# Performance work log

Hardware: AMD Instinct MI355X
Metric: run time of the kernel (lower is better)

## Reference

```python
import jax, jax.numpy as jnp
import numpy as np

V, FN, CIN, HID, PTS = 50000, 100000, 3, 256, 10000
TEMP = 0.1
EPS = 1e-20


def line_mesh_graph(f, Vn):
    # f: [F,3] int triangles. Build the 'line mesh': one node per unique mesh edge.
    fe = jnp.concatenate([f[:, :2], f[:, 1:], f[:, jnp.array([2, 0])]], 0)  # [3F,2]
    fe = jnp.sort(fe, axis=1)
    keys = fe[:, 0] * Vn + fe[:, 1]                       # [3F] unique key per undirected edge
    ukeys, inv = jnp.unique(keys, return_inverse=True)
    edge_node = jnp.stack([ukeys // Vn, ukeys % Vn], -1)  # [E,2] endpoints of each edge-node
    E = ukeys.shape[0]
    feid = inv.reshape(3, -1).T                           # [F,3] edge-node id per face edge
    # line-graph connectivity: edges of the same face are mutual neighbors, plus self-loops
    srcs, dsts = [], []
    for i, j in ((0, 1), (1, 0), (1, 2), (2, 1), (2, 0), (0, 2)):
        srcs.append(feid[:, i]); dsts.append(feid[:, j])
    loop = jnp.arange(E)
    edge = jnp.stack([jnp.concatenate(srcs + [loop]), jnp.concatenate(dsts + [loop])], 0)  # [2,NE]
    return edge, edge_node, keys


def gsn_conv(x, edge, Ws, Wn, b):
    # GSNConv stand-in: self transform + mean-aggregated neighbor transform
    s, d = edge[0], edge[1]
    N = x.shape[0]
    deg = jax.ops.segment_sum(jnp.ones_like(s, x.dtype), d, num_segments=N)
    agg = jax.ops.segment_sum(x[s], d, num_segments=N) / jnp.clip(deg, 1.0)[:, None]
    return x @ Ws + agg @ Wn + b


def gumbel_mask(logits, temperature, num, key):
    U = jax.random.uniform(key, logits.shape)
    g = -jnp.log(-jnp.log(U + EPS) + EPS)
    y = jax.nn.softmax((logits + g) / temperature, -1)[:, 0]  # [E]
    _, ind = jax.lax.top_k(y, num)
    y_hard = jnp.zeros_like(y).at[ind].set(1.0)
    mask = jax.lax.stop_gradient(y_hard - y) + y              # straight-through one-hot
    return mask, y_hard == 1.0


def mesh_collapse(f, keys, pool_edge, Vn):
    # Vectorized replacement of the per-pool-edge python loop: hash-join pooled edge keys
    # against all 3F face-edge keys via sorted search.
    PE = pool_edge.shape[0]
    pool_idx = jnp.arange(Vn, Vn + PE)
    edge_keys = keys.reshape(3, -1).T                     # [F,3] (cols: e01,e12,e20)
    pk = pool_edge[:, 0] * Vn + pool_edge[:, 1]
    order = jnp.argsort(pk); pks = pk[order]
    flat = edge_keys.reshape(-1)
    pos = jnp.clip(jnp.searchsorted(pks, flat), 0, PE - 1)
    found = pks[pos] == flat
    pei = jnp.where(found, pool_idx[order[pos]], -1).reshape(-1, 3)  # pool_edge_idx [F,3]
    fm = found.reshape(-1, 3)
    pen = fm.sum(1)                                       # pool_edge_num per face
    psi = (fm * jnp.arange(3)).sum(1)                     # pool_start_idx per face
    vv = jnp.stack([f[:, 0], pei[:, 0], f[:, 1], pei[:, 1], f[:, 2], pei[:, 2]], -1)
    nf0 = f[pen == 0]
    fv1 = vv[pen == 1]; s1 = psi[pen == 1]
    fv1 = jnp.concatenate([fv1[s1 == 0], jnp.roll(fv1[s1 == 1], -2, 1), jnp.roll(fv1[s1 == 2], 2, 1)], 0)
    nf1 = jnp.concatenate([jnp.stack([fv1[:, 0], fv1[:, 1], fv1[:, 4]], -1),
                           jnp.stack([fv1[:, 1], fv1[:, 2], fv1[:, 4]], -1)], 0)
    fv2 = vv[pen == 2]; s2 = psi[pen == 2]
    fv2 = jnp.concatenate([fv2[s2 == 1], jnp.roll(fv2[s2 == 2], 2, 1), jnp.roll(fv2[s2 == 3], -2, 1)], 0)
    nf2 = jnp.concatenate([jnp.stack([fv2[:, 0], fv2[:, 1], fv2[:, 4]], -1),
                           jnp.stack([fv2[:, 1], fv2[:, 2], fv2[:, 3]], -1),
                           jnp.stack([fv2[:, 1], fv2[:, 3], fv2[:, 4]], -1)], 0)
    fv3 = vv[pen == 3]
    nf3 = jnp.concatenate([jnp.stack([fv3[:, 0], fv3[:, 1], fv3[:, 5]], -1),
                           jnp.stack([fv3[:, 1], fv3[:, 2], fv3[:, 3]], -1),
                           jnp.stack([fv3[:, 1], fv3[:, 3], fv3[:, 5]], -1),
                           jnp.stack([fv3[:, 3], fv3[:, 4], fv3[:, 5]], -1)], 0)
    new_faces = jnp.concatenate([nf0, nf1, nf2, nf3], 0)
    ne = jnp.concatenate([new_faces[:, :2], new_faces[:, 1:], new_faces[:, jnp.array([2, 0])]], 0)
    ai = jnp.arange(Vn + PE)
    ne = jnp.concatenate([jnp.stack([ai, ai], -1), ne], 0)
    return new_faces, ne.T


def setup_inputs():
    key = jax.random.key(0)
    ks = jax.random.split(key, 10)
    s1 = 1.0 / np.sqrt(CIN); s2 = 1.0 / np.sqrt(HID)
    return {
        'input': jax.random.normal(ks[0], (1, V, CIN), jnp.float32),
        'face': jax.random.randint(ks[1], (1, FN, 3), 0, V),
        'coord': jax.random.normal(ks[2], (1, V, 3), jnp.float32),
        'detail_points': jax.random.normal(ks[3], (1, PTS, 3), jnp.float32),
        'div': 5,
        'W1s': jax.random.normal(ks[4], (CIN, HID), jnp.float32) * s1,
        'W1n': jax.random.normal(ks[5], (CIN, HID), jnp.float32) * s1,
        'b1': jnp.zeros((HID,), jnp.float32),
        'W2s': jax.random.normal(ks[6], (HID, 2), jnp.float32) * s2,
        'W2n': jax.random.normal(ks[7], (HID, 2), jnp.float32) * s2,
        'b2': jnp.zeros((2,), jnp.float32),
    }


def reference(input, face, coord, detail_points, div, W1s, W1n, b1, W2s, W2n, b2):
    # B=1 (data-dependent per-sample output sizes make batch stacking only valid then)
    x0, f = input[0], face[0]
    Vn = x0.shape[0]
    edge, edge_node, keys = line_mesh_graph(f, Vn)
    xe = 0.5 * (x0[edge_node[:, 0]] + x0[edge_node[:, 1]])   # edge-node features [E,C]
    h = jax.nn.relu(gsn_conv(xe, edge, W1s, W1n, b1))
    out = jax.nn.sigmoid(gsn_conv(h, edge, W2s, W2n, b2))    # [E,2]
    mask, pool_ind = gumbel_mask(out, TEMP, out.shape[0] // div, jax.random.key(42))
    pool_edge = edge_node[pool_ind]                          # [PE,2]
    new_faces, new_edges = mesh_collapse(f, keys, pool_edge, Vn)
    return edge_node[None], new_faces[None], new_edges[None], mask[None]
```

## Files before the change

### kernel.cpp

```cpp
#include <hip/hip_runtime.h>
#include <stdint.h>

typedef uint32_t u32;
typedef uint64_t u64;

#define VN 50000
#define FN 100000
#define K3F 300000
#define EMAX 300000
#define NB1 1172
#define NBC 98
#define NBH 293
#define NBS 293

#define W_A      0u
#define W_B      300000u
#define W_PA     600000u
#define W_PB     900000u
#define W_RANKU  1200000u
#define W_UKEYS  1500000u
#define W_SEGOFF 1800000u
#define W_FEID   2100004u
#define W_XE     2400004u
#define W_PK     3300004u
#define W_P      3400004u
#define W_Q      4000004u
#define W_Y      4600004u
#define W_YMAP   4900004u
#define W_T64    5200004u
#define W_SEL    5800068u
#define W_SELR   6100068u
#define W_CAT    6400068u
#define W_CATR   6500068u
#define W_NFI    6600068u
#define W_HIST   7800068u
#define W_SUMS   8100100u
#define W_CATH   8104196u
#define W_SCAL   8105220u

#define S_E 0
#define S_NUM 1
#define S_PFX 2
#define S_KREM 3
#define S_TU 4
#define S_R 5
#define S_NF 6
#define S_NEN 7
#define S_O1 8
#define S_O2 9
#define S_O3 10
#define S_RS 16
#define S_GS 24
#define S_GP 32

__device__ __forceinline__ void tf2x32(u32 x0, u32 x1, u32& o0, u32& o1) {
  const u32 ks0 = 0u, ks1 = 42u, ks2 = 0x1BD11BDAu ^ 0u ^ 42u;
  x0 += ks0; x1 += ks1;
#define TFR(r) { x0 += x1; x1 = (x1<<(r))|(x1>>(32-(r))); x1 ^= x0; }
  TFR(13) TFR(15) TFR(26) TFR(6)   x0 += ks1; x1 += ks2 + 1u;
  TFR(17) TFR(29) TFR(16) TFR(24)  x0 += ks2; x1 += ks0 + 2u;
  TFR(13) TFR(15) TFR(26) TFR(6)   x0 += ks0; x1 += ks1 + 3u;
  TFR(17) TFR(29) TFR(16) TFR(24)  x0 += ks1; x1 += ks2 + 4u;
  TFR(13) TFR(15) TFR(26) TFR(6)   x0 += ks2; x1 += ks0 + 5u;
#undef TFR
  o0 = x0; o1 = x1;
}

__global__ void scan_blocks(const u32* __restrict__ in, u32* __restrict__ out,
                            u32* __restrict__ sums, int n) {
  __shared__ u32 lds[256];
  int t = threadIdx.x;
  int base = blockIdx.x*1024 + t*4;
  u32 v[4]; u32 tot = 0;
  for (int k = 0; k < 4; ++k) { v[k] = (base+k < n) ? in[base+k] : 0u; tot += v[k]; }
  lds[t] = tot; __syncthreads();
  for (int o = 1; o < 256; o <<= 1) {
    u32 x = (t >= o) ? lds[t-o] : 0u; __syncthreads();
    lds[t] += x; __syncthreads();
  }
  u32 excl = lds[t] - tot;
  if (t == 255) sums[blockIdx.x] = lds[255];
  u32 run = excl;
  for (int k = 0; k < 4; ++k) { if (base+k < n) out[base+k] = run; run += v[k]; }
}

__global__ void scan_flagblocks(const u32* __restrict__ sk, u32* __restrict__ out,
                                u32* __restrict__ sums, int n) {
  __shared__ u32 lds[256];
  int t = threadIdx.x;
  int base = blockIdx.x*1024 + t*4;
  u32 v[4]; u32 tot = 0;
  for (int k = 0; k < 4; ++k) {
    int i = base + k;
    u32 f = 0;
    if (i < n) f = (i == 0 || sk[i-1] != sk[i]) ? 1u : 0u;
    v[k] = f; tot += f;
  }
  lds[t] = tot; __syncthreads();
  for (int o = 1; o < 256; o <<= 1) {
    u32 x = (t >= o) ? lds[t-o] : 0u; __syncthreads();
    lds[t] += x; __syncthreads();
  }
  u32 excl = lds[t] - tot;
  if (t == 255) sums[blockIdx.x] = lds[255];
  u32 run = excl;
  for (int k = 0; k < 4; ++k) { if (base+k < n) out[base+k] = run; run += v[k]; }
}

__global__ void scan_sums(u32* __restrict__ s, int nb) {
  __shared__ u32 lds[256];
  __shared__ u32 carry;
  int t = threadIdx.x;
  if (t == 0) carry = 0;
  __syncthreads();
  for (int base = 0; base < nb; base += 1024) {
    int idx = base + t*4;
    u32 v[4]; u32 tot = 0;
    for (int k = 0; k < 4; ++k) { v[k] = (idx+k < nb) ? s[idx+k] : 0u; tot += v[k]; }
    lds[t] = tot; __syncthreads();
    for (int o = 1; o < 256; o <<= 1) {
      u32 x = (t >= o) ? lds[t-o] : 0u; __syncthreads();
      lds[t] += x; __syncthreads();
    }
    u32 excl = lds[t] - tot;
    u32 ctot = lds[255];
    u32 c = carry;
    __syncthreads();
    u32 run = c + excl;
    for (int k = 0; k < 4; ++k) { if (idx+k < nb) s[idx+k] = run; run += v[k]; }
    if (t == 0) carry = c + ctot;
    __syncthreads();
  }
}

__global__ void scan64_src(const u32* __restrict__ ymap, const u32* __restrict__ scal,
                           u64* __restrict__ part, u64* __restrict__ sums) {
  __shared__ u64 lds[256];
  int t = threadIdx.x;
  int base = blockIdx.x*1024 + t*4;
  int E = (int)scal[S_E];
  u32 TU = scal[S_TU];
  u64 v[4]; u64 tot = 0;
  for (int k = 0; k < 4; ++k) {
    int e = base + k;
    u64 val = 0;
    if (e < E) {
      u32 u = ymap[e];
      if (u > TU) val = 1ull;
      else if (u == TU) val = 1ull << 32;
    }
    v[k] = val; tot += val;
  }
  lds[t] = tot; __syncthreads();
  for (int o = 1; o < 256; o <<= 1) {
    u64 x = (t >= o) ? lds[t-o] : 0ull; __syncthreads();
    lds[t] += x; __syncthreads();
  }
  u64 excl = lds[t] - tot;
  if (t == 255) sums[blockIdx.x] = lds[255];
  u64 run = excl;
  for (int k = 0; k < 4; ++k) { part[base+k] = run; run += v[k]; }
}

__global__ void scan64_sums(u64* __restrict__ s, int nb) {
  __shared__ u64 lds[256];
  int t = threadIdx.x;
  int idx = t*4;
  u64 v[4]; u64 tot = 0;
  for (int k = 0; k < 4; ++k) { v[k] = (idx+k < nb) ? s[idx+k] : 0ull; tot += v[k]; }
  lds[t] = tot; __syncthreads();
  for (int o = 1; o < 256; o <<= 1) {
    u64 x = (t >= o) ? lds[t-o] : 0ull; __syncthreads();
    lds[t] += x; __syncthreads();
  }
  u64 excl = lds[t] - tot;
  u64 run = excl;
  for (int k = 0; k < 4; ++k) { if (idx+k < nb) s[idx+k] = run; run += v[k]; }
}

__global__ void k_sel2(const u32* __restrict__ ymap, const u64* __restrict__ part,
                       const u64* __restrict__ sums, const u32* __restrict__ scal,
                       u32* __restrict__ sel, u32* __restrict__ selr) {
  int e = blockIdx.x*256 + threadIdx.x;
  if (e >= EMAX) return;
  int E = (int)scal[S_E];
  u32 TU = scal[S_TU], R = scal[S_R];
  u64 pre = part[e] + sums[e>>10];
  u32 GTpre = (u32)pre, TIEpre = (u32)(pre >> 32);
  u32 v = 0;
  if (e < E) {
    u32 u = ymap[e];
    v = (u > TU) || (u == TU && TIEpre < R);
  }
  sel[e] = v ? 1u : 0u;
  selr[e] = GTpre + min(TIEpre, R);
}

__global__ void k_rhist(const u32* __restrict__ keys, u32* __restrict__ hist,
                        int n, int shift, int nb) {
  __shared__ u32 h[256];
  int t = threadIdx.x;
  h[t] = 0; __syncthreads();
  int i = blockIdx.x*256 + t;
  if (i < n) atomicAdd(&h[(keys[i]>>shift)&255u], 1u);
  __syncthreads();
  hist[(u32)t*nb + blockIdx.x] = h[t];
}

__global__ void k_rscat(const u32* __restrict__ keys, const u32* __restrict__ pay,
                        u32* __restrict__ okeys, u32* __restrict__ opay,
                        const u32* __restrict__ hist, const u32* __restrict__ sums,
                        int n, int shift, int nb) {
  __shared__ u64 ball[4][8];
  __shared__ u64 vmask[4];
  int t = threadIdx.x, w = t>>6, lane = t&63;
  int i = blockIdx.x*256 + t;
  bool valid = i < n;
  u32 k = valid ? keys[i] : 0u;
  u32 d = (k>>shift)&255u;
  for (int bit = 0; bit < 8; ++bit) {
    u64 bm = __ballot(valid && ((d>>bit)&1u));
    if (lane == 0) ball[w][bit] = bm;
  }
  u64 vb = __ballot(valid ? 1 : 0);
  if (lane == 0) vmask[w] = vb;
  __syncthreads();
  if (valid) {
    u32 rank = 0;
    for (int ww = 0; ww < w; ++ww) {
      u64 m = vmask[ww];
      for (int bit = 0; bit < 8; ++bit) { u64 bb = ball[ww][bit]; m &= ((d>>bit)&1u) ? bb : ~bb; }
      rank += (u32)__popcll(m);
    }
    u64 m = vmask[w];
    for (int bit = 0; bit < 8; ++bit) { u64 bb = ball[w][bit]; m &= ((d>>bit)&1u) ? bb : ~bb; }
    rank += (u32)__popcll(m & ((1ull<<lane)-1ull));
    u32 h = d*(u32)nb + blockIdx.x;
    u32 pos = hist[h] + sums[h>>10] + rank;
    okeys[pos] = k;
    opay[pos] = pay[i];
  }
}

__global__ void k_keys(const int* __restrict__ face, u32* __restrict__ keys,
                       u32* __restrict__ pay) {
  int i = blockIdx.x*256 + threadIdx.x;
  if (i >= K3F) return;
  int s = i / FN, f = i - s*FN;
  int v0 = face[f*3 + s];
  int v1 = face[f*3 + (s == 2 ? 0 : s+1)];
  int a = min(v0, v1), b = max(v0, v1);
  u32 key = (u32)a * (u32)VN + (u32)b;
  keys[i] = key ^ 0x80000000u;
  pay[i] = (u32)i;
}

__global__ void k_uwrite(const u32* __restrict__ sk, const u32* __restrict__ rankp,
                         const u32* __restrict__ sums, const u32* __restrict__ pay,
                         u32* __restrict__ ukeys, u32* __restrict__ segoff,
                         u32* __restrict__ feid,
                         u32* __restrict__ scal, const int* __restrict__ divp) {
  int p = blockIdx.x*256 + threadIdx.x;
  if (p >= K3F) return;
  u32 cur = sk[p];
  u32 fl = (p == 0 || sk[p-1] != cur) ? 1u : 0u;
  u32 rk = rankp[p] + sums[p>>10];
  if (fl) { ukeys[rk] = cur; segoff[rk] = (u32)p; }
  u32 id = rk - 1u + fl;
  u32 i = pay[p];
  u32 s = i / FN, f = i - s*FN;
  feid[f*3 + s] = id;
  if (p == K3F-1) {
    u32 E = rk + fl;
    scal[S_E] = E; scal[S_NUM] = E / (u32)divp[0];
    segoff[E] = (u32)K3F;
  }
}

__global__ void k_ennode(const u32* __restrict__ ukeys, const u32* __restrict__ scal,
                         const float* __restrict__ x,
                         float* __restrict__ xe, float* __restrict__ dout) {
  int e = blockIdx.x*256 + threadIdx.x;
  if (e >= (int)scal[S_E]) return;
  int k = (int)(ukeys[e] ^ 0x80000000u);
  long long kk = (long long)k;
  long long qq = (kk - (kk < 0 ? (long long)(VN-1) : 0ll)) / VN;
  int q = (int)qq;
  int r = (int)(kk - qq * VN);
  dout[2*e]   = (float)q;
  dout[2*e+1] = (float)r;
  u32 i0 = (u32)(q < 0 ? q + VN : q);
  u32 i1 = (u32)r;
  for (int c = 0; c < 3; ++c) xe[e*3+c] = 0.5f*(x[i0*3+c] + x[i1*3+c]);
}

__global__ void k_pack(const float* __restrict__ W1s, const float* __restrict__ W1n,
                       const float* __restrict__ b1,
                       const float* __restrict__ W2s, const float* __restrict__ W2n,
                       float* __restrict__ pk) {
  int h = threadIdx.x;
  if (h >= 256) return;
  float* p = pk + h*12;
  p[0] = W1s[h]; p[1] = W1s[256+h]; p[2] = W1s[512+h];
  p[3] = W1n[h]; p[4] = W1n[256+h]; p[5] = W1n[512+h];
  p[6] = b1[h];
  p[7] = W2s[2*h]; p[8] = W2s[2*h+1];
  p[9] = W2n[2*h]; p[10] = W2n[2*h+1];
  p[11] = 0.0f;
}

__device__ __forceinline__ void agg_neighbors(int e, u32 st, u32 en,
                                              const u32* __restrict__ pay,
                                              const u32* __restrict__ feid,
                                              const float* __restrict__ v, int stride,
                                              float* acc0, float* acc1, float* acc2) {
  const int sslot[6] = {0,1,1,2,2,0};
  const int dslot[6] = {1,0,2,1,0,2};
  float c0 = 0.f, c1 = 0.f, c2 = 0.f;
  for (int b = 0; b < 6; ++b) {
    int j = dslot[b], isl = sslot[b];
    for (u32 p = st; p < en; ++p) {
      u32 i = pay[p];
      u32 s = i / FN;
      if ((int)s == j) {
        u32 f = i - s*FN;
        u32 u = feid[f*3 + isl];
        c0 += v[u*stride]; c1 += v[u*stride+1]; if (stride == 3) c2 += v[u*stride+2];
      }
    }
  }
  c0 += v[e*stride]; c1 += v[e*stride+1]; if (stride == 3) c2 += v[e*stride+2];
  *acc0 = c0; *acc1 = c1; *acc2 = c2;
}

__global__ void k_l12(const float* __restrict__ xe, const u32* __restrict__ segoff,
                      const u32* __restrict__ pay, const u32* __restrict__ feid,
                      const u32* __restrict__ scal, const float* __restrict__ pk,
                      float* __restrict__ P, float* __restrict__ Q) {
  int e = blockIdx.x*256 + threadIdx.x;
  if (e >= (int)scal[S_E]) return;
  u32 st = segoff[e], en = segoff[e+1];
  float c0, c1, c2;
  agg_neighbors(e, st, en, pay, feid, xe, 3, &c0, &c1, &c2);
  float x0 = xe[e*3], x1 = xe[e*3+1], x2 = xe[e*3+2];
  float dg = (float)(2u*(en - st) + 1u);
  float m0 = c0/dg, m1 = c1/dg, m2 = c2/dg;
  float p0 = 0.f, p1 = 0.f, q0 = 0.f, q1 = 0.f;
#pragma unroll 8
  for (int hh = 0; hh < 256; ++hh) {
    const float* w = pk + hh*12;
    float s1 = x0*w[0] + x1*w[1] + x2*w[2];
    float s2 = m0*w[3] + m1*w[4] + m2*w[5];
    float h = fmaxf(s1 + s2 + w[6], 0.0f);
    p0 += h*w[7];  p1 += h*w[8];
    q0 += h*w[9];  q1 += h*w[10];
  }
  P[2*e] = p0; P[2*e+1] = p1; Q[2*e] = q0; Q[2*e+1] = q1;
}

__global__ void k_scores(const float* __restrict__ P, const float* __restrict__ Q,
                         const u32* __restrict__ segoff, const u32* __restrict__ pay,
                         const u32* __restrict__ feid,
                         const float* __restrict__ b2, const u32* __restrict__ scal,
                         float* __restrict__ Y, u32* __restrict__ ymap) {
  int e = blockIdx.x*256 + threadIdx.x;
  u32 E = scal[S_E];
  if (e >= (int)E) return;
  u32 st = segoff[e], en = segoff[e+1];
  float a0, a1, dummy;
  agg_neighbors(e, st, en, pay, feid, Q, 2, &a0, &a1, &dummy);
  float dg = (float)(2u*(en - st) + 1u);
  float z0 = P[2*e]   + a0/dg + b2[0];
  float z1 = P[2*e+1] + a1/dg + b2[1];
  float l0 = 1.0f/(1.0f + expf(-z0));
  float l1 = 1.0f/(1.0f + expf(-z1));
  u32 g0b, g1b;
  { u32 o0,o1; tf2x32(0u, 2u*(u32)e,      o0, o1); g0b = o0 ^ o1; }
  { u32 o0,o1; tf2x32(0u, 2u*(u32)e + 1u, o0, o1); g1b = o0 ^ o1; }
  float U0 = __uint_as_float((g0b>>9) | 0x3f800000u) - 1.0f;
  float U1 = __uint_as_float((g1b>>9) | 0x3f800000u) - 1.0f;
  float g0 = -logf(-logf(U0 + 1e-20f) + 1e-20f);
  float g1 = -logf(-logf(U1 + 1e-20f) + 1e-20f);
  float A0 = (l0 + g0)/0.1f;
  float A1 = (l1 + g1)/0.1f;
  float mx = fmaxf(A0, A1);
  float e0 = expf(A0-mx), e1 = expf(A1-mx);
  float y = e0/(e0+e1);
  Y[e] = y;
  ymap[e] = __float_as_uint(y) | 0x80000000u;
}

__global__ void k_tkinit(u32* __restrict__ scal, u32* __restrict__ hist) {
  int t = threadIdx.x;
  if (t < 256) hist[t] = 0u;
  if (t == 0) { scal[S_PFX] = 0u; scal[S_KREM] = scal[S_NUM]; }
}

__global__ void k_tkhist(const u32* __restrict__ ymap, const u32* __restrict__ scal,
                         u32* __restrict__ hist, int byte) {
  __shared__ u32 h[256];
  int t = threadIdx.x;
  h[t] = 0u; __syncthreads();
  int E = (int)scal[S_E];
  u32 pfx = scal[S_PFX];
  int base = blockIdx.x*1024;
  for (int k = 0; k < 4; ++k) {
    int e = base + k*256 + t;
    if (e < E) {
      u32 u = ymap[e];
      bool match = (byte == 3) || ((u >> ((byte+1)*8)) == pfx);
      if (match) atomicAdd(&h[(u >> (byte*8)) & 255u], 1u);
    }
  }
  __syncthreads();
  u32 c = h[t];
  if (c) atomicAdd(&hist[t], c);
}

__global__ void k_tksel(u32* __restrict__ scal, u32* __restrict__ hist, int byte) {
  __shared__ u32 s2[256];
  __shared__ u32 chosen_s;
  int t = threadIdx.x;
  u32 v = hist[t];
  hist[t] = 0u;
  s2[t] = v;
  if (t == 0) chosen_s = 0u;
  __syncthreads();
  for (int o = 1; o < 256; o <<= 1) {
    u32 x = (t + o < 256) ? s2[t+o] : 0u; __syncthreads();
    s2[t] += x; __syncthreads();
  }
  u32 krem = scal[S_KREM];
  if (s2[t] >= krem) atomicMax(&chosen_s, (u32)t);
  __syncthreads();
  if (t == 0) {
    u32 chosen = chosen_s;
    u32 sufnext = (chosen < 255u) ? s2[chosen+1] : 0u;
    u32 newkrem = krem - sufnext;
    u32 pfx = (scal[S_PFX] << 8) | chosen;
    scal[S_PFX] = pfx; scal[S_KREM] = newkrem;
    if (byte == 0) { scal[S_TU] = pfx; scal[S_R] = newkrem; }
  }
}

__global__ void k_cat(const u32* __restrict__ feid, const u32* __restrict__ sel,
                      u32* __restrict__ cat) {
  int f = blockIdx.x*256 + threadIdx.x;
  if (f >= FN) return;
  u32 m0 = sel[feid[f*3]], m1 = sel[feid[f*3+1]], m2 = sel[feid[f*3+2]];
  u32 pen = m0 + m1 + m2;
  u32 psi = m1 + 2u*m2;
  u32 c = (pen == 0) ? 0u : (pen == 1) ? (1u+psi) : (pen == 2) ? (3u+psi) : 7u;
  cat[f] = c;
}

__global__ void k_cathist(const u32* __restrict__ cat, u32* __restrict__ ch) {
  __shared__ u32 h[8];
  int t = threadIdx.x;
  if (t < 8) h[t] = 0u;
  __syncthreads();
  int base = blockIdx.x*1024 + t*4;
  for (int k = 0; k < 4; ++k) if (base+k < FN) atomicAdd(&h[cat[base+k]], 1u);
  __syncthreads();
  if (t < 8) ch[(u32)t*NBC + blockIdx.x] = h[t];
}

__global__ void k_catoff(u32* __restrict__ ch, u32* __restrict__ scal) {
  __shared__ u32 lds[256];
  __shared__ u32 ex[1024];
  int t = threadIdx.x;
  u32 v[4]; u32 tot = 0;
  for (int k = 0; k < 4; ++k) {
    int i = t*4 + k;
    u32 x = (i < 8*NBC) ? ch[i] : 0u;
    v[k] = x; tot += x;
  }
  lds[t] = tot; __syncthreads();
  for (int o = 1; o < 256; o <<= 1) {
    u32 x = (t >= o) ? lds[t-o] : 0u; __syncthreads();
    lds[t] += x; __syncthreads();
  }
  u32 excl = lds[t] - tot;
  u32 run = excl;
  for (int k = 0; k < 4; ++k) { ex[t*4+k] = run; run += v[k]; }
  __syncthreads();
  for (int k = 0; k < 4; ++k) {
    int i = t*4 + k;
    if (i < 8*NBC) ch[i] = ex[i];
  }
  if (t == 0) {
    u32 total = lds[255];
    u32 bnd[9];
    for (int c = 0; c < 8; ++c) bnd[c] = ex[c*NBC];
    bnd[8] = total;
    u32 tot8[8];
    for (int c = 0; c < 8; ++c) tot8[c] = bnd[c+1] - bnd[c];
    u32 n0 = tot8[0], n1 = tot8[1]+tot8[2]+tot8[3], n2 = tot8[4]+tot8[5]+tot8[6], n3 = tot8[7];
    u32 NF = n0 + 2u*n1 + 3u*n2 + 4u*n3;
    u32 E = scal[S_E], num = scal[S_NUM];
    u32 NEn = (u32)VN + num + 3u*NF;
    scal[S_NF] = NF; scal[S_NEN] = NEn;
    scal[S_O1] = 2u*E;
    scal[S_O2] = 2u*E + 3u*NF;
    scal[S_O3] = 2u*E + 3u*NF + 2u*NEn;
    u32 RS[8] = {0u, n0,n0,n0, n0+2u*n1, n0+2u*n1, n0+2u*n1, n0+2u*n1+3u*n2};
    u32 GS[8] = {0u, n1,n1,n1, n2,n2,n2, n3};
    u32 GP[8] = {0u, n0,n0,n0, n0+n1, n0+n1, n0+n1, n0+n1+n2};
    for (int i = 0; i < 8; ++i) { scal[S_RS+i] = RS[i]; scal[S_GS+i] = GS[i]; scal[S_GP+i] = GP[i]; }
  }
}

__global__ void k_catrank(const u32* __restrict__ cat, const u32* __restrict__ ch,
                          u32* __restrict__ cr) {
  __shared__ u32 lds[256];
  int t = threadIdx.x;
  int base = blockIdx.x*1024 + t*4;
  u32 cc[4], loc[4];
  u32 cnt[8] = {0,0,0,0,0,0,0,0};
  for (int k = 0; k < 4; ++k) {
    int i = base + k;
    if (i < FN) { u32 c = cat[i]; cc[k] = c; loc[k] = cnt[c]++; }
    else cc[k] = 8u;
  }
  u32 tb[8];
  for (int c = 0; c < 8; ++c) {
    lds[t] = cnt[c]; __syncthreads();
    for (int o = 1; o < 256; o <<= 1) {
      u32 x = (t >= o) ? lds[t-o] : 0u; __syncthreads();
      lds[t] += x; __syncthreads();
    }
    tb[c] = lds[t] - cnt[c];
    __syncthreads();
  }
  for (int k = 0; k < 4; ++k) {
    int i = base + k;
    if (i < FN) { u32 c = cc[k]; cr[i] = ch[c*NBC + blockIdx.x] + tb[c] + loc[k]; }
  }
}

__global__ void k_wfaces(const int* __restrict__ face, const u32* __restrict__ cat,
                         const u32* __restrict__ cr, const u32* __restrict__ feid,
                         const u32* __restrict__ selr, const u32* __restrict__ scal,
                         int* __restrict__ nfi, float* __restrict__ dout) {
  int f = blockIdx.x*256 + threadIdx.x;
  if (f >= FN) return;
  const int nfc[8] = {1,2,2,2,3,3,3,4};
  const int tri[8][4][3] = {
    {{0,2,4},{0,0,0},{0,0,0},{0,0,0}},
    {{0,1,4},{1,2,4},{0,0,0},{0,0,0}},
    {{2,3,0},{3,4,0},{0,0,0},{0,0,0}},
    {{4,5,2},{5,0,2},{0,0,0},{0,0,0}},
    {{0,1,4},{1,2,3},{1,3,4},{0,0,0}},
    {{4,5,2},{5,0,1},{5,1,2},{0,0,0}},
    {{2,3,0},{3,4,5},{3,5,0},{0,0,0}},
    {{0,1,5},{1,2,3},{1,3,5},{3,4,5}}};
  u32 c = cat[f];
  int cv[6];
  cv[0] = face[f*3];   cv[2] = face[f*3+1]; cv[4] = face[f*3+2];
  cv[1] = VN + (int)selr[feid[f*3]];
  cv[3] = VN + (int)selr[feid[f*3+1]];
  cv[5] = VN + (int)selr[feid[f*3+2]];
  u32 g  = cr[f] - scal[S_GP + c];
  u32 o1 = scal[S_O1];
  for (int j = 0; j < nfc[c]; ++j) {
    u32 row = scal[S_RS + c] + (u32)j*scal[S_GS + c] + g;
    for (int m = 0; m < 3; ++m) {
      int v = cv[tri[c][j][m]];
      nfi[row*3 + m] = v;
      dout[o1 + row*3 + m] = (float)v;
    }
  }
}

__global__ void k_wne(const int* __restrict__ nfi, const u32* __restrict__ scal,
                      float* __restrict__ dout) {
  int i = blockIdx.x*256 + threadIdx.x;
  u32 NEn = scal[S_NEN];
  if (i >= (int)NEn) return;
  u32 NF = scal[S_NF];
  u32 Vp = (u32)VN + scal[S_NUM];
  u32 o2 = scal[S_O2];
  int a, b;
  if ((u32)i < Vp) { a = i; b = i; }
  else {
    u32 j = (u32)i - Vp;
    u32 blk = j / NF, r = j - blk*NF;
    int i0 = (blk == 0) ? 0 : (blk == 1) ? 1 : 2;
    int i1 = (blk == 0) ? 1 : (blk == 1) ? 2 : 0;
    a = nfi[r*3 + i0]; b = nfi[r*3 + i1];
  }
  dout[o2 + i] = (float)a;
  dout[o2 + NEn + i] = (float)b;
}

__global__ void k_wmask(const u32* __restrict__ sel, const float* __restrict__ Y,
                        const u32* __restrict__ scal, float* __restrict__ dout) {
  int e = blockIdx.x*256 + threadIdx.x;
  if (e >= (int)scal[S_E]) return;
  float y = Y[e];
  float yh = sel[e] ? 1.0f : 0.0f;
  dout[scal[S_O3] + e] = (yh - y) + y;
}

static void radix_pass(u32* kin, u32* pin, u32* kout, u32* pout, u32* hist, u32* sums,
                       int n, int nb, int shift, hipStream_t st) {
  k_rhist<<<nb, 256, 0, st>>>(kin, hist, n, shift, nb);
  int nscan = nb*256;
  int nbs = (nscan + 1023)/1024;
  scan_blocks<<<nbs, 256, 0, st>>>(hist, hist, sums, nscan);
  scan_sums<<<1, 256, 0, st>>>(sums, nbs);
  k_rscat<<<nb, 256, 0, st>>>(kin, pin, kout, pout, hist, sums, n, shift, nb);
}

extern "C" void kernel_launch(void* const* d_in, const int* in_sizes, int n_in,
                              void* d_out, int out_size, void* d_ws, size_t ws_size,
                              hipStream_t stream) {
  const float* x    = (const float*)d_in[0];
  const int*   face = (const int*)d_in[1];
  const int*   divp = (const int*)d_in[4];
  const float* W1s  = (const float*)d_in[5];
  const float* W1n  = (const float*)d_in[6];
  const float* b1   = (const float*)d_in[7];
  const float* W2s  = (const float*)d_in[8];
  const float* W2n  = (const float*)d_in[9];
  const float* b2   = (const float*)d_in[10];
  float* out = (float*)d_out;
  u32* W = (u32*)d_ws;

  u32 *A = W+W_A, *B = W+W_B, *PA = W+W_PA, *PB = W+W_PB;
  u32 *RK = W+W_RANKU, *UK = W+W_UKEYS;
  u32 *HIST = W+W_HIST, *SUMS = W+W_SUMS, *SCAL = W+W_SCAL;
  u64 *T64 = (u64*)(W+W_T64);
  u64 *SUMS64 = (u64*)(W+W_SUMS);

  k_pack<<<1, 256, 0, stream>>>(W1s, W1n, b1, W2s, W2n, (float*)(W+W_PK));

  k_keys<<<NB1, 256, 0, stream>>>(face, A, PA);
  radix_pass(A, PA, B, PB, HIST, SUMS, K3F, NB1,  0, stream);
  radix_pass(B, PB, A, PA, HIST, SUMS, K3F, NB1,  8, stream);
  radix_pass(A, PA, B, PB, HIST, SUMS, K3F, NB1, 16, stream);
  radix_pass(B, PB, A, PA, HIST, SUMS, K3F, NB1, 24, stream);
  scan_flagblocks<<<NBS, 256, 0, stream>>>(A, RK, SUMS, K3F);
  scan_sums<<<1, 256, 0, stream>>>(SUMS, NBS);
  k_uwrite<<<NB1, 256, 0, stream>>>(A, RK, SUMS, PA, UK, W+W_SEGOFF, W+W_FEID, SCAL, divp);

  k_ennode<<<NB1, 256, 0, stream>>>(UK, SCAL, x, (float*)(W+W_XE), out);

  k_l12<<<NB1, 256, 0, stream>>>((float*)(W+W_XE), W+W_SEGOFF, PA, W+W_FEID, SCAL,
                                 (float*)(W+W_PK), (float*)(W+W_P), (float*)(W+W_Q));
  k_scores<<<NB1, 256, 0, stream>>>((float*)(W+W_P), (float*)(W+W_Q), W+W_SEGOFF, PA,
                                    W+W_FEID, b2, SCAL, (float*)(W+W_Y), W+W_YMAP);

  k_tkinit<<<1, 256, 0, stream>>>(SCAL, HIST);
  for (int byte = 3; byte >= 0; --byte) {
    k_tkhist<<<NBH, 256, 0, stream>>>(W+W_YMAP, SCAL, HIST, byte);
    k_tksel<<<1, 256, 0, stream>>>(SCAL, HIST, byte);
  }
  scan64_src<<<NBS, 256, 0, stream>>>(W+W_YMAP, SCAL, T64, SUMS64);
  scan64_sums<<<1, 256, 0, stream>>>(SUMS64, NBS);
  k_sel2<<<NB1, 256, 0, stream>>>(W+W_YMAP, T64, SUMS64, SCAL, W+W_SEL, W+W_SELR);

  k_cat<<<391, 256, 0, stream>>>(W+W_FEID, W+W_SEL, W+W_CAT);
  k_cathist<<<NBC, 256, 0, stream>>>(W+W_CAT, W+W_CATH);
  k_catoff<<<1, 256, 0, stream>>>(W+W_CATH, SCAL);
  k_catrank<<<NBC, 256, 0, stream>>>(W+W_CAT, W+W_CATH, W+W_CATR);
  k_wfaces<<<391, 256, 0, stream>>>(face, W+W_CAT, W+W_CATR, W+W_FEID, W+W_SELR, SCAL,
                                    (int*)(W+W_NFI), out);
  k_wne<<<5118, 256, 0, stream>>>((int*)(W+W_NFI), SCAL, out);
  k_wmask<<<NB1, 256, 0, stream>>>(W+W_SEL, (float*)(W+W_Y), SCAL, out);
}
```

Measured before the change: 329.2 us.

## Pack radix keys with payloads and fuse small kernels to cut launches

Keys and payload indices are packed into one 64-bit word, so each radix scatter does a single store instead of two. The first pass histogram moves into the key-generation kernel, which also absorbs the weight packing. Edge-node feature computation moves into the unique-write kernel. The top-k histogram and select kernels merge into one per round using a last-block-done atomic counter, and the category and category-histogram kernels are fused. This removes many small launches and extra passes, at the cost of 64-bit memory traffic in the sort and a grid-wide completion counter that relies on threadfence ordering.

```diff
diff --git a/kernel.cpp b/kernel.cpp
--- a/kernel.cpp
+++ b/kernel.cpp
@@ -13,30 +13,29 @@
 #define NBH 293
 #define NBS 293
 
-#define W_A      0u
-#define W_B      300000u
-#define W_PA     600000u
-#define W_PB     900000u
+#define W_KPA    0u
+#define W_KPB    600000u
 #define W_RANKU  1200000u
-#define W_UKEYS  1500000u
-#define W_SEGOFF 1800000u
-#define W_FEID   2100004u
-#define W_XE     2400004u
-#define W_PK     3300004u
-#define W_P      3400004u
-#define W_Q      4000004u
-#define W_Y      4600004u
-#define W_YMAP   4900004u
-#define W_T64    5200004u
-#define W_SEL    5800068u
-#define W_SELR   6100068u
-#define W_CAT    6400068u
-#define W_CATR   6500068u
-#define W_NFI    6600068u
-#define W_HIST   7800068u
-#define W_SUMS   8100100u
-#define W_CATH   8104196u
-#define W_SCAL   8105220u
+#define W_SEGOFF 1500000u
+#define W_FEID   1800004u
+#define W_XE     2100004u
+#define W_PK     3000004u
+#define W_P      3100004u
+#define W_Q      3700004u
+#define W_Y      4300004u
+#define W_YMAP   4600004u
+#define W_T64    4900004u
+#define W_SEL    5500068u
+#define W_SELR   5800068u
+#define W_CAT    6100068u
+#define W_CATR   6200068u
+#define W_NFI    6300068u
+#define W_HIST   7500068u
+#define W_SUMS   7800100u
+#define W_CATH   7804196u
+#define W_TKH    7805220u
+#define W_DONE   7805476u
+#define W_SCAL   7805504u
 
 #define S_E 0
 #define S_NUM 1
@@ -84,7 +83,7 @@
   for (int k = 0; k < 4; ++k) { if (base+k < n) out[base+k] = run; run += v[k]; }
 }
 
-__global__ void scan_flagblocks(const u32* __restrict__ sk, u32* __restrict__ out,
+__global__ void scan_flagblocks(const u64* __restrict__ kp, u32* __restrict__ out,
                                 u32* __restrict__ sums, int n) {
   __shared__ u32 lds[256];
   int t = threadIdx.x;
@@ -93,7 +92,7 @@
   for (int k = 0; k < 4; ++k) {
     int i = base + k;
     u32 f = 0;
-    if (i < n) f = (i == 0 || sk[i-1] != sk[i]) ? 1u : 0u;
+    if (i < n) f = (i == 0 || (u32)(kp[i-1]>>32) != (u32)(kp[i]>>32)) ? 1u : 0u;
     v[k] = f; tot += f;
   }
   lds[t] = tot; __syncthreads();
@@ -196,28 +195,27 @@
   selr[e] = GTpre + min(TIEpre, R);
 }
 
-__global__ void k_rhist(const u32* __restrict__ keys, u32* __restrict__ hist,
-                        int n, int shift, int nb) {
+__global__ void k_rhist(const u64* __restrict__ kp, u32* __restrict__ hist,
+                        int shift, int nb) {
   __shared__ u32 h[256];
   int t = threadIdx.x;
   h[t] = 0; __syncthreads();
   int i = blockIdx.x*256 + t;
-  if (i < n) atomicAdd(&h[(keys[i]>>shift)&255u], 1u);
+  if (i < K3F) atomicAdd(&h[((u32)(kp[i]>>32) >> shift) & 255u], 1u);
   __syncthreads();
   hist[(u32)t*nb + blockIdx.x] = h[t];
 }
 
-__global__ void k_rscat(const u32* __restrict__ keys, const u32* __restrict__ pay,
-                        u32* __restrict__ okeys, u32* __restrict__ opay,
+__global__ void k_rscat(const u64* __restrict__ kp, u64* __restrict__ okp,
                         const u32* __restrict__ hist, const u32* __restrict__ sums,
-                        int n, int shift, int nb) {
+                        int shift, int nb) {
   __shared__ u64 ball[4][8];
   __shared__ u64 vmask[4];
   int t = threadIdx.x, w = t>>6, lane = t&63;
   int i = blockIdx.x*256 + t;
-  bool valid = i < n;
-  u32 k = valid ? keys[i] : 0u;
-  u32 d = (k>>shift)&255u;
+  bool valid = i < K3F;
+  u64 v = valid ? kp[i] : 0ull;
+  u32 d = ((u32)(v>>32) >> shift) & 255u;
   for (int bit = 0; bit < 8; ++bit) {
     u64 bm = __ballot(valid && ((d>>bit)&1u));
     if (lane == 0) ball[w][bit] = bm;
@@ -237,80 +235,86 @@
     rank += (u32)__popcll(m & ((1ull<<lane)-1ull));
     u32 h = d*(u32)nb + blockIdx.x;
     u32 pos = hist[h] + sums[h>>10] + rank;
-    okeys[pos] = k;
-    opay[pos] = pay[i];
-  }
-}
-
-__global__ void k_keys(const int* __restrict__ face, u32* __restrict__ keys,
-                       u32* __restrict__ pay) {
-  int i = blockIdx.x*256 + threadIdx.x;
-  if (i >= K3F) return;
-  int s = i / FN, f = i - s*FN;
-  int v0 = face[f*3 + s];
-  int v1 = face[f*3 + (s == 2 ? 0 : s+1)];
-  int a = min(v0, v1), b = max(v0, v1);
-  u32 key = (u32)a * (u32)VN + (u32)b;
-  keys[i] = key ^ 0x80000000u;
-  pay[i] = (u32)i;
-}
-
-__global__ void k_uwrite(const u32* __restrict__ sk, const u32* __restrict__ rankp,
-                         const u32* __restrict__ sums, const u32* __restrict__ pay,
-                         u32* __restrict__ ukeys, u32* __restrict__ segoff,
-                         u32* __restrict__ feid,
+    okp[pos] = v;
+  }
+}
+
+__global__ void k_keys(const int* __restrict__ face,
+                       const float* __restrict__ W1s, const float* __restrict__ W1n,
+                       const float* __restrict__ b1,
+                       const float* __restrict__ W2s, const float* __restrict__ W2n,
+                       float* __restrict__ pk,
+                       u64* __restrict__ kp, u32* __restrict__ hist,
+                       u32* __restrict__ tkh, u32* __restrict__ done) {
+  __shared__ u32 h[256];
+  int t = threadIdx.x;
+  h[t] = 0;
+  __syncthreads();
+  if (blockIdx.x == 0) {
+    tkh[t] = 0u;
+    if (t < 16) done[t] = 0u;
+    float* p = pk + t*12;
+    p[0] = W1s[t]; p[1] = W1s[256+t]; p[2] = W1s[512+t];
+    p[3] = W1n[t]; p[4] = W1n[256+t]; p[5] = W1n[512+t];
+    p[6] = b1[t];
+    p[7] = W2s[2*t]; p[8] = W2s[2*t+1];
+    p[9] = W2n[2*t]; p[10] = W2n[2*t+1];
+    p[11] = 0.0f;
+  }
+  int i = blockIdx.x*256 + t;
+  if (i < K3F) {
+    int s = i / FN, f = i - s*FN;
+    int v0 = face[f*3 + s];
+    int v1 = face[f*3 + (s == 2 ? 0 : s+1)];
+    int a = min(v0, v1), b = max(v0, v1);
+    u32 key = ((u32)a * (u32)VN + (u32)b) ^ 0x80000000u;
+    kp[i] = ((u64)key << 32) | (u32)i;
+    atomicAdd(&h[key & 255u], 1u);
+  }
+  __syncthreads();
+  hist[(u32)t*NB1 + blockIdx.x] = h[t];
+}
+
+__global__ void k_uwrite(const u64* __restrict__ kp, const u32* __restrict__ rankp,
+                         const u32* __restrict__ sums, const float* __restrict__ x,
+                         u32* __restrict__ segoff, u32* __restrict__ feid,
+                         float* __restrict__ xe, float* __restrict__ dout,
                          u32* __restrict__ scal, const int* __restrict__ divp) {
   int p = blockIdx.x*256 + threadIdx.x;
   if (p >= K3F) return;
-  u32 cur = sk[p];
-  u32 fl = (p == 0 || sk[p-1] != cur) ? 1u : 0u;
+  u64 v = kp[p];
+  u32 cur = (u32)(v >> 32);
+  u32 fl = (p == 0 || (u32)(kp[p-1] >> 32) != cur) ? 1u : 0u;
   u32 rk = rankp[p] + sums[p>>10];
-  if (fl) { ukeys[rk] = cur; segoff[rk] = (u32)p; }
+  if (fl) {
+    u32 e = rk;
+    segoff[e] = (u32)p;
+    int k = (int)(cur ^ 0x80000000u);
+    long long kk = (long long)k;
+    long long qq = (kk - (kk < 0 ? (long long)(VN-1) : 0ll)) / VN;
+    int q = (int)qq;
+    int r = (int)(kk - qq * VN);
+    dout[2*e]   = (float)q;
+    dout[2*e+1] = (float)r;
+    u32 i0 = (u32)(q < 0 ? q + VN : q);
+    u32 i1 = (u32)r;
+    for (int c = 0; c < 3; ++c) xe[e*3+c] = 0.5f*(x[i0*3+c] + x[i1*3+c]);
+  }
   u32 id = rk - 1u + fl;
-  u32 i = pay[p];
+  u32 i = (u32)v;
   u32 s = i / FN, f = i - s*FN;
   feid[f*3 + s] = id;
   if (p == K3F-1) {
     u32 E = rk + fl;
-    scal[S_E] = E; scal[S_NUM] = E / (u32)divp[0];
+    u32 num = E / (u32)divp[0];
+    scal[S_E] = E; scal[S_NUM] = num;
     segoff[E] = (u32)K3F;
-  }
-}
-
-__global__ void k_ennode(const u32* __restrict__ ukeys, const u32* __restrict__ scal,
-                         const float* __restrict__ x,
-                         float* __restrict__ xe, float* __restrict__ dout) {
-  int e = blockIdx.x*256 + threadIdx.x;
-  if (e >= (int)scal[S_E]) return;
-  int k = (int)(ukeys[e] ^ 0x80000000u);
-  long long kk = (long long)k;
-  long long qq = (kk - (kk < 0 ? (long long)(VN-1) : 0ll)) / VN;
-  int q = (int)qq;
-  int r = (int)(kk - qq * VN);
-  dout[2*e]   = (float)q;
-  dout[2*e+1] = (float)r;
-  u32 i0 = (u32)(q < 0 ? q + VN : q);
-  u32 i1 = (u32)r;
-  for (int c = 0; c < 3; ++c) xe[e*3+c] = 0.5f*(x[i0*3+c] + x[i1*3+c]);
-}
-
-__global__ void k_pack(const float* __restrict__ W1s, const float* __restrict__ W1n,
-                       const float* __restrict__ b1,
-                       const float* __restrict__ W2s, const float* __restrict__ W2n,
-                       float* __restrict__ pk) {
-  int h = threadIdx.x;
-  if (h >= 256) return;
-  float* p = pk + h*12;
-  p[0] = W1s[h]; p[1] = W1s[256+h]; p[2] = W1s[512+h];
-  p[3] = W1n[h]; p[4] = W1n[256+h]; p[5] = W1n[512+h];
-  p[6] = b1[h];
-  p[7] = W2s[2*h]; p[8] = W2s[2*h+1];
-  p[9] = W2n[2*h]; p[10] = W2n[2*h+1];
-  p[11] = 0.0f;
+    scal[S_PFX] = 0u; scal[S_KREM] = num;
+  }
 }
 
 __device__ __forceinline__ void agg_neighbors(int e, u32 st, u32 en,
-                                              const u32* __restrict__ pay,
+                                              const u64* __restrict__ kp,
                                               const u32* __restrict__ feid,
                                               const float* __restrict__ v, int stride,
                                               float* acc0, float* acc1, float* acc2) {
@@ -320,7 +324,7 @@
   for (int b = 0; b < 6; ++b) {
     int j = dslot[b], isl = sslot[b];
     for (u32 p = st; p < en; ++p) {
-      u32 i = pay[p];
+      u32 i = (u32)kp[p];
       u32 s = i / FN;
       if ((int)s == j) {
         u32 f = i - s*FN;
@@ -334,14 +338,14 @@
 }
 
 __global__ void k_l12(const float* __restrict__ xe, const u32* __restrict__ segoff,
-                      const u32* __restrict__ pay, const u32* __restrict__ feid,
+                      const u64* __restrict__ kp, const u32* __restrict__ feid,
                       const u32* __restrict__ scal, const float* __restrict__ pk,
                       float* __restrict__ P, float* __restrict__ Q) {
   int e = blockIdx.x*256 + threadIdx.x;
   if (e >= (int)scal[S_E]) return;
   u32 st = segoff[e], en = segoff[e+1];
   float c0, c1, c2;
-  agg_neighbors(e, st, en, pay, feid, xe, 3, &c0, &c1, &c2);
+  agg_neighbors(e, st, en, kp, feid, xe, 3, &c0, &c1, &c2);
   float x0 = xe[e*3], x1 = xe[e*3+1], x2 = xe[e*3+2];
   float dg = (float)(2u*(en - st) + 1u);
   float m0 = c0/dg, m1 = c1/dg, m2 = c2/dg;
@@ -359,7 +363,7 @@
 }
 
 __global__ void k_scores(const float* __restrict__ P, const float* __restrict__ Q,
-                         const u32* __restrict__ segoff, const u32* __restrict__ pay,
+                         const u32* __restrict__ segoff, const u64* __restrict__ kp,
                          const u32* __restrict__ feid,
                          const float* __restrict__ b2, const u32* __restrict__ scal,
                          float* __restrict__ Y, u32* __restrict__ ymap) {
@@ -368,7 +372,7 @@
   if (e >= (int)E) return;
   u32 st = segoff[e], en = segoff[e+1];
   float a0, a1, dummy;
-  agg_neighbors(e, st, en, pay, feid, Q, 2, &a0, &a1, &dummy);
+  agg_neighbors(e, st, en, kp, feid, Q, 2, &a0, &a1, &dummy);
   float dg = (float)(2u*(en - st) + 1u);
   float z0 = P[2*e]   + a0/dg + b2[0];
   float z1 = P[2*e+1] + a1/dg + b2[1];
@@ -390,17 +394,16 @@
   ymap[e] = __float_as_uint(y) | 0x80000000u;
 }
 
-__global__ void k_tkinit(u32* __restrict__ scal, u32* __restrict__ hist) {
-  int t = threadIdx.x;
-  if (t < 256) hist[t] = 0u;
-  if (t == 0) { scal[S_PFX] = 0u; scal[S_KREM] = scal[S_NUM]; }
-}
-
-__global__ void k_tkhist(const u32* __restrict__ ymap, const u32* __restrict__ scal,
-                         u32* __restrict__ hist, int byte) {
+__global__ void k_tkround(const u32* __restrict__ ymap, u32* __restrict__ scal,
+                          u32* __restrict__ hist, u32* __restrict__ done, int byte) {
   __shared__ u32 h[256];
-  int t = threadIdx.x;
-  h[t] = 0u; __syncthreads();
+  __shared__ u32 s2[256];
+  __shared__ u32 chosen_s;
+  __shared__ u32 lastflag;
+  int t = threadIdx.x;
+  h[t] = 0u;
+  if (t == 0) lastflag = 0u;
+  __syncthreads();
   int E = (int)scal[S_E];
   u32 pfx = scal[S_PFX];
   int base = blockIdx.x*1024;
@@ -415,14 +418,16 @@
   __syncthreads();
   u32 c = h[t];
   if (c) atomicAdd(&hist[t], c);
-}
-
-__global__ void k_tksel(u32* __restrict__ scal, u32* __restrict__ hist, int byte) {
-  __shared__ u32 s2[256];
-  __shared__ u32 chosen_s;
-  int t = threadIdx.x;
-  u32 v = hist[t];
-  hist[t] = 0u;
+  __syncthreads();
+  if (t == 0) {
+    __threadfence();
+    u32 old = atomicAdd(&done[byte], 1u);
+    if (old == gridDim.x - 1u) lastflag = 1u;
+  }
+  __syncthreads();
+  if (!lastflag) return;
+  __threadfence();
+  u32 v = atomicExch(&hist[t], 0u);
   s2[t] = v;
   if (t == 0) chosen_s = 0u;
   __syncthreads();
@@ -437,30 +442,30 @@
     u32 chosen = chosen_s;
     u32 sufnext = (chosen < 255u) ? s2[chosen+1] : 0u;
     u32 newkrem = krem - sufnext;
-    u32 pfx = (scal[S_PFX] << 8) | chosen;
-    scal[S_PFX] = pfx; scal[S_KREM] = newkrem;
-    if (byte == 0) { scal[S_TU] = pfx; scal[S_R] = newkrem; }
-  }
-}
-
-__global__ void k_cat(const u32* __restrict__ feid, const u32* __restrict__ sel,
-                      u32* __restrict__ cat) {
-  int f = blockIdx.x*256 + threadIdx.x;
-  if (f >= FN) return;
-  u32 m0 = sel[feid[f*3]], m1 = sel[feid[f*3+1]], m2 = sel[feid[f*3+2]];
-  u32 pen = m0 + m1 + m2;
-  u32 psi = m1 + 2u*m2;
-  u32 c = (pen == 0) ? 0u : (pen == 1) ? (1u+psi) : (pen == 2) ? (3u+psi) : 7u;
-  cat[f] = c;
-}
-
-__global__ void k_cathist(const u32* __restrict__ cat, u32* __restrict__ ch) {
+    u32 npfx = (scal[S_PFX] << 8) | chosen;
+    scal[S_PFX] = npfx; scal[S_KREM] = newkrem;
+    if (byte == 0) { scal[S_TU] = npfx; scal[S_R] = newkrem; }
+  }
+}
+
+__global__ void k_catfused(const u32* __restrict__ feid, const u32* __restrict__ sel,
+                           u32* __restrict__ cat, u32* __restrict__ ch) {
   __shared__ u32 h[8];
   int t = threadIdx.x;
   if (t < 8) h[t] = 0u;
   __syncthreads();
   int base = blockIdx.x*1024 + t*4;
-  for (int k = 0; k < 4; ++k) if (base+k < FN) atomicAdd(&h[cat[base+k]], 1u);
+  for (int k = 0; k < 4; ++k) {
+    int f = base + k;
+    if (f < FN) {
+      u32 m0 = sel[feid[f*3]], m1 = sel[feid[f*3+1]], m2 = sel[feid[f*3+2]];
+      u32 pen = m0 + m1 + m2;
+      u32 psi = m1 + 2u*m2;
+      u32 c = (pen == 0) ? 0u : (pen == 1) ? (1u+psi) : (pen == 2) ? (3u+psi) : 7u;
+      cat[f] = c;
+      atomicAdd(&h[c], 1u);
+    }
+  }
   __syncthreads();
   if (t < 8) ch[(u32)t*NBC + blockIdx.x] = h[t];
 }
@@ -602,14 +607,12 @@
   dout[scal[S_O3] + e] = (yh - y) + y;
 }
 
-static void radix_pass(u32* kin, u32* pin, u32* kout, u32* pout, u32* hist, u32* sums,
-                       int n, int nb, int shift, hipStream_t st) {
-  k_rhist<<<nb, 256, 0, st>>>(kin, hist, n, shift, nb);
-  int nscan = nb*256;
-  int nbs = (nscan + 1023)/1024;
-  scan_blocks<<<nbs, 256, 0, st>>>(hist, hist, sums, nscan);
-  scan_sums<<<1, 256, 0, st>>>(sums, nbs);
-  k_rscat<<<nb, 256, 0, st>>>(kin, pin, kout, pout, hist, sums, n, shift, nb);
+static void radix_pass(u32* hist, u32* sums, u64* kin, u64* kout, int shift,
+                       bool do_hist, hipStream_t st) {
+  if (do_hist) k_rhist<<<NB1, 256, 0, st>>>(kin, hist, shift, NB1);
+  scan_blocks<<<NBS, 256, 0, st>>>(hist, hist, sums, NB1*256);
+  scan_sums<<<1, 256, 0, st>>>(sums, NBS);
+  k_rscat<<<NB1, 256, 0, st>>>(kin, kout, hist, sums, shift, NB1);
 }
 
 extern "C" void kernel_launch(void* const* d_in, const int* in_sizes, int n_in,
@@ -627,41 +630,36 @@
   float* out = (float*)d_out;
   u32* W = (u32*)d_ws;
 
-  u32 *A = W+W_A, *B = W+W_B, *PA = W+W_PA, *PB = W+W_PB;
-  u32 *RK = W+W_RANKU, *UK = W+W_UKEYS;
+  u64 *KPA = (u64*)(W+W_KPA), *KPB = (u64*)(W+W_KPB);
+  u32 *RK = W+W_RANKU;
   u32 *HIST = W+W_HIST, *SUMS = W+W_SUMS, *SCAL = W+W_SCAL;
+  u32 *TKH = W+W_TKH, *DONE = W+W_DONE;
   u64 *T64 = (u64*)(W+W_T64);
   u64 *SUMS64 = (u64*)(W+W_SUMS);
 
-  k_pack<<<1, 256, 0, stream>>>(W1s, W1n, b1, W2s, W2n, (float*)(W+W_PK));
-
-  k_keys<<<NB1, 256, 0, stream>>>(face, A, PA);
-  radix_pass(A, PA, B, PB, HIST, SUMS, K3F, NB1,  0, stream);
-  radix_pass(B, PB, A, PA, HIST, SUMS, K3F, NB1,  8, stream);
-  radix_pass(A, PA, B, PB, HIST, SUMS, K3F, NB1, 16, stream);
-  radix_pass(B, PB, A, PA, HIST, SUMS, K3F, NB1, 24, stream);
-  scan_flagblocks<<<NBS, 256, 0, stream>>>(A, RK, SUMS, K3F);
+  k_keys<<<NB1, 256, 0, stream>>>(face, W1s, W1n, b1, W2s, W2n, (float*)(W+W_PK),
+                                  KPA, HIST, TKH, DONE);
+  radix_pass(HIST, SUMS, KPA, KPB,  0, false, stream);
+  radix_pass(HIST, SUMS, KPB, KPA,  8, true,  stream);
+  radix_pass(HIST, SUMS, KPA, KPB, 16, true,  stream);
+  radix_pass(HIST, SUMS, KPB, KPA, 24, true,  stream);
+  scan_flagblocks<<<NBS, 256, 0, stream>>>(KPA, RK, SUMS, K3F);
   scan_sums<<<1, 256, 0, stream>>>(SUMS, NBS);
-  k_uwrite<<<NB1, 256, 0, stream>>>(A, RK, SUMS, PA, UK, W+W_SEGOFF, W+W_FEID, SCAL, divp);
-
-  k_ennode<<<NB1, 256, 0, stream>>>(UK, SCAL, x, (float*)(W+W_XE), out);
-
-  k_l12<<<NB1, 256, 0, stream>>>((float*)(W+W_XE), W+W_SEGOFF, PA, W+W_FEID, SCAL,
+  k_uwrite<<<NB1, 256, 0, stream>>>(KPA, RK, SUMS, x, W+W_SEGOFF, W+W_FEID,
+                                    (float*)(W+W_XE), out, SCAL, divp);
+
+  k_l12<<<NB1, 256, 0, stream>>>((float*)(W+W_XE), W+W_SEGOFF, KPA, W+W_FEID, SCAL,
                                  (float*)(W+W_PK), (float*)(W+W_P), (float*)(W+W_Q));
-  k_scores<<<NB1, 256, 0, stream>>>((float*)(W+W_P), (float*)(W+W_Q), W+W_SEGOFF, PA,
+  k_scores<<<NB1, 256, 0, stream>>>((float*)(W+W_P), (float*)(W+W_Q), W+W_SEGOFF, KPA,
                                     W+W_FEID, b2, SCAL, (float*)(W+W_Y), W+W_YMAP);
 
-  k_tkinit<<<1, 256, 0, stream>>>(SCAL, HIST);
-  for (int byte = 3; byte >= 0; --byte) {
-    k_tkhist<<<NBH, 256, 0, stream>>>(W+W_YMAP, SCAL, HIST, byte);
-    k_tksel<<<1, 256, 0, stream>>>(SCAL, HIST, byte);
-  }
+  for (int byte = 3; byte >= 0; --byte)
+    k_tkround<<<NBH, 256, 0, stream>>>(W+W_YMAP, SCAL, TKH, DONE, byte);
   scan64_src<<<NBS, 256, 0, stream>>>(W+W_YMAP, SCAL, T64, SUMS64);
   scan64_sums<<<1, 256, 0, stream>>>(SUMS64, NBS);
   k_sel2<<<NB1, 256, 0, stream>>>(W+W_YMAP, T64, SUMS64, SCAL, W+W_SEL, W+W_SELR);
 
-  k_cat<<<391, 256, 0, stream>>>(W+W_FEID, W+W_SEL, W+W_CAT);
-  k_cathist<<<NBC, 256, 0, stream>>>(W+W_CAT, W+W_CATH);
+  k_catfused<<<NBC, 256, 0, stream>>>(W+W_FEID, W+W_SEL, W+W_CAT, W+W_CATH);
   k_catoff<<<1, 256, 0, stream>>>(W+W_CATH, SCAL);
   k_catrank<<<NBC, 256, 0, stream>>>(W+W_CAT, W+W_CATH, W+W_CATR);
   k_wfaces<<<391, 256, 0, stream>>>(face, W+W_CAT, W+W_CATR, W+W_FEID, W+W_SELR, SCAL,
```

New measurement: 320.0 us. -2.8%, faster.
